# Performance work log

Measured on AMD Instinct MI355X. Metric: run time of the kernel, lower is better.

The kernel has to match this reference:

```python
import jax, jax.numpy as jnp
import numpy as np


def setup_inputs() -> dict:
    key = jax.random.key(0)
    B, N, C, H, W = 2, 512, 256, 128, 224
    ks = jax.random.split(key, 6)
    point_features = jax.random.normal(ks[0], (B, N, C), dtype=jnp.float32)
    gd = jax.random.uniform(ks[1], (B, N, 14), dtype=jnp.float32)
    # realistic radar positions (meters): X in [-10,10], Y in [-2,2], Z (depth) in [1,41]
    pos = jnp.stack([(gd[..., 0] - 0.5) * 20.0,
                     (gd[..., 1] - 0.5) * 4.0,
                     gd[..., 2] * 40.0 + 1.0], axis=-1)
    gd = gd.at[..., :3].set(pos)
    # sigmas in original-image pixels, in [0, 20] so some exceed 1 after scaling
    gd = gd.at[..., 5:7].set(gd[..., 5:7] * 20.0)
    # nuScenes-like intrinsics for a 1600x900 camera
    K = jnp.array([[500.0, 0.0, 800.0], [0.0, 500.0, 450.0], [0.0, 0.0, 1.0]], dtype=jnp.float32)
    intrinsic = jnp.tile(K[None], (B, 1, 1))
    sc = 1.0 / np.sqrt(C)
    W1 = jax.random.normal(ks[2], (C, C), dtype=jnp.float32) * sc
    b1 = jax.random.normal(ks[3], (C,), dtype=jnp.float32) * 0.01
    W2 = jax.random.normal(ks[4], (C, C), dtype=jnp.float32) * sc
    b2 = jax.random.normal(ks[5], (C,), dtype=jnp.float32) * 0.01
    return {"point_features": point_features, "gaussian_data": gd, "intrinsic": intrinsic,
            "W1": W1, "b1": b1, "W2": W2, "b2": b2, "H": H, "W": W}


def reference(point_features, gaussian_data, intrinsic, W1, b1, W2, b2, H, W):
    pf, gd, K = point_features, gaussian_data, intrinsic
    B, N, C = pf.shape
    # positions / sigmas are consumed via numpy/.item() in the original -> constants w.r.t. autodiff
    pos = jax.lax.stop_gradient(gd[..., :3])          # (B,N,3)
    sig_x = jax.lax.stop_gradient(gd[..., 5])         # (B,N)
    sig_y = jax.lax.stop_gradient(gd[..., 6])         # (B,N)
    wts = gd[..., 12]                                  # (B,N) differentiable weights

    valid = pos[..., 2] > 0.1
    # project to image plane
    p2h = jnp.einsum('bij,bnj->bni', K, pos)           # (B,N,3)
    p2 = p2h[..., :2] / (p2h[..., 2:3] + 1e-6)
    scale_x = W / K[:, 0, 2] / 2.0                     # (B,)
    scale_y = H / K[:, 1, 2] / 2.0
    cx = p2[..., 0] * scale_x[:, None]                 # (B,N)
    cy = p2[..., 1] * scale_y[:, None]
    inb = (cx >= 0) & (cx < W) & (cy >= 0) & (cy < H)
    active = (valid & inb).astype(pf.dtype)            # (B,N)

    sxv = jnp.maximum(sig_x * scale_x[:, None], 1.0)   # (B,N)
    syv = jnp.maximum(sig_y * scale_y[:, None], 1.0)

    xs = jnp.arange(W, dtype=pf.dtype)
    ys = jnp.arange(H, dtype=pf.dtype)
    dist_x = ((xs[None, None, :] - cx[..., None]) / sxv[..., None]) ** 2  # (B,N,W)
    dist_y = ((ys[None, None, :] - cy[..., None]) / syv[..., None]) ** 2  # (B,N,H)
    dist = dist_y[..., :, None] + dist_x[..., None, :]                    # (B,N,H,W)
    gw = jnp.exp(-0.5 * dist) * (dist < 9.0).astype(pf.dtype)
    gw = gw * (wts * active)[..., None, None]                             # masked splat weights

    # feature transform: Linear -> ReLU -> Linear
    h = jax.nn.relu(pf @ W1.T + b1) @ W2.T + b2                           # (B,N,C)

    feature_map = jnp.einsum('bnhw,bnc->bchw', gw, h)                     # (B,C,H,W)
    avg_sigma = 0.5 * (sxv + syv)                                         # (B,N)
    uncertainty_map = jnp.einsum('bnhw,bn->bhw', gw, avg_sigma)[:, None]  # (B,1,H,W)
    density_map = jnp.clip(jnp.sum(gw, axis=1), 1e-6, None)[:, None]      # (B,1,H,W)

    return feature_map / density_map, uncertainty_map / density_map, density_map
```

## Files before the change

### kernel.cpp

```cpp
#include <hip/hip_runtime.h>
#include <math.h>

#define PTS 8
#define PX 16
#define CH 8
#define NTX 14
#define NBLK 1536

__global__ void prep_kernel(const float* __restrict__ gd,
                            const float* __restrict__ Kmat,
                            float4* __restrict__ bbox,
                            float4* __restrict__ prm,
                            int N, int B, float Wf, float Hf) {
  int i = blockIdx.x * blockDim.x + threadIdx.x;
  if (i >= B * N) return;
  int b = i / N;
  const float* g = gd + (size_t)i * 14;
  float X = g[0], Y = g[1], Z = g[2];
  float sigx = g[5], sigy = g[6], wt = g[12];
  const float* K = Kmat + (size_t)b * 9;
  float p0 = K[0]*X + K[1]*Y + K[2]*Z;
  float p1 = K[3]*X + K[4]*Y + K[5]*Z;
  float p2 = K[6]*X + K[7]*Y + K[8]*Z;
  float denom = p2 + 1e-6f;
  float p2x = p0 / denom, p2y = p1 / denom;
  float scale_x = Wf / K[2] * 0.5f;
  float scale_y = Hf / K[5] * 0.5f;
  float cx = p2x * scale_x;
  float cy = p2y * scale_y;
  bool valid = Z > 0.1f;
  bool inb = (cx >= 0.f) && (cx < Wf) && (cy >= 0.f) && (cy < Hf);
  bool active = valid && inb;
  float sxv = fmaxf(sigx * scale_x, 1.f);
  float syv = fmaxf(sigy * scale_y, 1.f);
  float wn = active ? wt : 0.f;
  float avg = 0.5f * (sxv + syv);
  if (active && wn != 0.f) {
    bbox[i] = make_float4(cx, cy, 3.f * sxv, 3.f * syv);
  } else {
    bbox[i] = make_float4(-1e30f, -1e30f, 0.f, 0.f);
  }
  prm[i] = make_float4(1.f / sxv, 1.f / syv, wn, avg);
}

__global__ __launch_bounds__(256, 2) void mlp_kernel(
    const float* __restrict__ pf, const float* __restrict__ W1,
    const float* __restrict__ b1, const float* __restrict__ W2,
    const float* __restrict__ b2, float* __restrict__ hout, int npts) {
  const int t = threadIdx.x;
  const int p0 = blockIdx.x * PTS;
  __shared__ __align__(16) float xs[PTS][256];

  const float4* pf4 = (const float4*)(pf + (size_t)p0 * 256);
  float4* xs4 = (float4*)&xs[0][0];
  #pragma unroll
  for (int i = 0; i < PTS * 64 / 256; ++i) xs4[t + 256 * i] = pf4[t + 256 * i];
  __syncthreads();

  float acc[PTS];
  float bb1 = b1[t];
  #pragma unroll
  for (int p = 0; p < PTS; ++p) acc[p] = bb1;
  const float* w1r = W1 + (size_t)t * 256;
  for (int k = 0; k < 256; k += 4) {
    float4 w = *(const float4*)(w1r + k);
    #pragma unroll
    for (int p = 0; p < PTS; ++p) {
      float4 x = *(const float4*)(&xs[p][k]);
      acc[p] += w.x * x.x + w.y * x.y + w.z * x.z + w.w * x.w;
    }
  }
  __syncthreads();
  #pragma unroll
  for (int p = 0; p < PTS; ++p) xs[p][t] = fmaxf(acc[p], 0.f);
  __syncthreads();

  float acc2[PTS];
  float bb2 = b2[t];
  #pragma unroll
  for (int p = 0; p < PTS; ++p) acc2[p] = bb2;
  const float* w2r = W2 + (size_t)t * 256;
  for (int k = 0; k < 256; k += 4) {
    float4 w = *(const float4*)(w2r + k);
    #pragma unroll
    for (int p = 0; p < PTS; ++p) {
      float4 x = *(const float4*)(&xs[p][k]);
      acc2[p] += w.x * x.x + w.y * x.y + w.z * x.z + w.w * x.w;
    }
  }
  #pragma unroll
  for (int p = 0; p < PTS; ++p)
    if (p0 + p < npts) hout[((size_t)(p0 + p)) * 256 + t] = acc2[p];
}

__global__ __launch_bounds__(256) void tilecull_kernel(
    const float4* __restrict__ bbox, int* __restrict__ tilelist,
    int* __restrict__ tilecnt, int N, int H, int W) {
  const int t = threadIdx.x;
  const int row = blockIdx.x;
  const int b = blockIdx.y;
  __shared__ int wcnt[4];
  __shared__ float xlo_s[512], xhi_s[512];
  __shared__ short gid_s[512];
  const float rf = (float)row;
  const float wmax = (float)(W - 1);
  const int lane = t & 63, wave = t >> 6;
  const unsigned long long lmask = (1ull << lane) - 1ull;
  const size_t bN = (size_t)b * N;

  int rowlen = 0;
  for (int gb = 0; gb < N; gb += 256) {
    int g = gb + t;
    bool f = false;
    float bxlo = 0.f, bxhi = 0.f;
    if (g < N) {
      float4 bb = bbox[bN + g];
      bxlo = bb.x - bb.z; bxhi = bb.x + bb.z;
      f = (bb.y - bb.w <= rf) && (bb.y + bb.w >= rf) &&
          (bxhi >= 0.f) && (bxlo <= wmax);
    }
    unsigned long long m = __ballot(f);
    if (lane == 0) wcnt[wave] = __popcll(m);
    __syncthreads();
    int pre = 0;
    #pragma unroll
    for (int wv = 0; wv < 4; ++wv) pre += (wv < wave) ? wcnt[wv] : 0;
    int tot = wcnt[0] + wcnt[1] + wcnt[2] + wcnt[3];
    if (f) {
      int idx = rowlen + pre + __popcll(m & lmask);
      gid_s[idx] = (short)g; xlo_s[idx] = bxlo; xhi_s[idx] = bxhi;
    }
    __syncthreads();
    rowlen += tot;
  }

  for (int tx = wave; tx < NTX; tx += 4) {
    const float txlo = (float)(tx * PX), txhi = txlo + (float)(PX - 1);
    const size_t tid = ((size_t)b * H + row) * NTX + tx;
    int* out = tilelist + tid * 512;
    int cnt = 0;
    for (int rb = 0; rb < rowlen; rb += 64) {
      int i = rb + lane;
      bool f = false; int g = 0;
      if (i < rowlen) {
        f = (xhi_s[i] >= txlo) && (xlo_s[i] <= txhi);
        g = gid_s[i];
      }
      unsigned long long m = __ballot(f);
      if (f) out[cnt + __popcll(m & lmask)] = g;
      cnt += __popcll(m);
    }
    if (lane == 0) tilecnt[tid] = cnt;
  }
}

__global__ __launch_bounds__(256) void splat_kernel(
    const float4* __restrict__ bbox, const float4* __restrict__ prm,
    const float* __restrict__ hfeat,
    const int* __restrict__ tilelist, const int* __restrict__ tilecnt,
    float* __restrict__ fout, float* __restrict__ unc_out,
    float* __restrict__ dens_out, int N, int C, int H, int W, int ntiles) {
  const int t = threadIdx.x;
  const int HW = H * W;

  __shared__ int glist[512];
  __shared__ __align__(16) float wlds[2][CH][PX];
  __shared__ __align__(16) float invd_s[PX];
  __shared__ float avgs_s[2][CH];

  const int cg = t >> 2, pq = t & 3;
  const int gi_w = t >> 4, j_w = t & 15;

  for (int tid = blockIdx.x; tid < ntiles; tid += NBLK) {
    const int tx = tid % NTX;
    const int rowb = tid / NTX;
    const int row = rowb % H;
    const int b = rowb / H;
    const int x0 = tx * PX;
    const size_t bN = (size_t)b * N;
    const float rf = (float)row;
    const float xlo = (float)x0;

    const int cnt = tilecnt[tid];
    __syncthreads();

    if (cnt == 0) {
      if (t < PX) {
        size_t pix = (size_t)b * HW + (size_t)row * W + x0 + t;
        dens_out[pix] = 1e-6f;
        unc_out[pix] = 0.f;
      }
      float4 z = make_float4(0.f, 0.f, 0.f, 0.f);
      float* fo = fout + ((size_t)(b * C + 4 * cg)) * HW + (size_t)row * W + x0 + 4 * pq;
      *(float4*)(fo)        = z;
      *(float4*)(fo + HW)   = z;
      *(float4*)(fo + 2*HW) = z;
      *(float4*)(fo + 3*HW) = z;
      continue;
    }

    for (int i = t; i < cnt; i += 256) glist[i] = tilelist[(size_t)tid * 512 + i];
    __syncthreads();

    float dreg = 0.f, ureg = 0.f;
    float4 a0 = make_float4(0.f,0.f,0.f,0.f), a1 = a0, a2 = a0, a3 = a0;
    float4 hvA[CH], hvB[CH];
    const int nchunk = (cnt + CH - 1) / CH;

#define HV8(HV, CB) do { \
    int gn_ = cnt - (CB); \
    _Pragma("unroll") \
    for (int gi = 0; gi < CH; ++gi) { \
      int idx_ = (CB) + gi; if (idx_ > cnt - 1) idx_ = cnt - 1; \
      HV[gi] = (gi < gn_) ? *(const float4*)(hfeat + (bN + glist[idx_]) * (size_t)C + 4 * cg) \
                          : make_float4(0.f, 0.f, 0.f, 0.f); \
    } } while (0)

#define WGT8(BUF, CB) do { \
    if (t < CH * PX) { \
      float w_ = 0.f, av_ = 0.f; \
      int gn_ = cnt - (CB); \
      if (gi_w < gn_) { \
        int g_ = glist[(CB) + gi_w]; \
        float4 bb_ = bbox[bN + g_]; \
        float4 pr_ = prm[bN + g_]; \
        float dx_ = (xlo + (float)j_w - bb_.x) * pr_.x; \
        float dy_ = (rf - bb_.y) * pr_.y; \
        float q_ = dx_ * dx_ + dy_ * dy_; \
        w_ = (q_ < 9.f) ? __expf(-0.5f * q_) * pr_.z : 0.f; \
        av_ = pr_.w; \
      } \
      wlds[BUF][gi_w][j_w] = w_; \
      if (j_w == 0) avgs_s[BUF][gi_w] = av_; \
    } } while (0)

#define DENS8(BUF, GC) do { \
    if (t < PX) { \
      for (int gi = 0; gi < (GC); ++gi) { \
        float w = wlds[BUF][gi][t]; \
        dreg += w; ureg += w * avgs_s[BUF][gi]; \
      } } } while (0)

#define FMA8(BUF, HV) do { \
    const float4* wr_ = (const float4*)&wlds[BUF][0][0]; \
    _Pragma("unroll") \
    for (int gi = 0; gi < CH; ++gi) { \
      float4 w = wr_[gi * 4 + pq]; \
      float4 h = HV[gi]; \
      a0.x += w.x*h.x; a0.y += w.y*h.x; a0.z += w.z*h.x; a0.w += w.w*h.x; \
      a1.x += w.x*h.y; a1.y += w.y*h.y; a1.z += w.z*h.y; a1.w += w.w*h.y; \
      a2.x += w.x*h.z; a2.y += w.y*h.z; a2.z += w.z*h.z; a2.w += w.w*h.z; \
      a3.x += w.x*h.w; a3.y += w.y*h.w; a3.z += w.z*h.w; a3.w += w.w*h.w; \
    } } while (0)

    HV8(hvA, 0);
    WGT8(0, 0);
    __syncthreads();
    for (int c = 0; c < nchunk; c += 2) {
      {
        const int gc = min(CH, cnt - c * CH);
        HV8(hvB, (c + 1) * CH);
        WGT8(1, (c + 1) * CH);
        DENS8(0, gc);
        FMA8(0, hvA);
        __syncthreads();
      }
      if (c + 1 < nchunk) {
        const int gc = min(CH, cnt - (c + 1) * CH);
        HV8(hvA, (c + 2) * CH);
        WGT8(0, (c + 2) * CH);
        DENS8(1, gc);
        FMA8(1, hvB);
        __syncthreads();
      }
    }

    if (t < PX) {
      float dc = fmaxf(dreg, 1e-6f);
      float inv = 1.f / dc;
      invd_s[t] = inv;
      size_t pix = (size_t)b * HW + (size_t)row * W + x0 + t;
      dens_out[pix] = dc;
      unc_out[pix] = ureg * inv;
    }
    __syncthreads();

    float4 iq = *(const float4*)&invd_s[4 * pq];
    float* fo = fout + ((size_t)(b * C + 4 * cg)) * HW + (size_t)row * W + x0 + 4 * pq;
    *(float4*)(fo)        = make_float4(a0.x*iq.x, a0.y*iq.y, a0.z*iq.z, a0.w*iq.w);
    *(float4*)(fo + HW)   = make_float4(a1.x*iq.x, a1.y*iq.y, a1.z*iq.z, a1.w*iq.w);
    *(float4*)(fo + 2*HW) = make_float4(a2.x*iq.x, a2.y*iq.y, a2.z*iq.z, a2.w*iq.w);
    *(float4*)(fo + 3*HW) = make_float4(a3.x*iq.x, a3.y*iq.y, a3.z*iq.z, a3.w*iq.w);

#undef HV8
#undef WGT8
#undef DENS8
#undef FMA8
  }
}

extern "C" void kernel_launch(void* const* d_in, const int* in_sizes, int n_in,
                              void* d_out, int out_size, void* d_ws, size_t ws_size,
                              hipStream_t stream) {
  const float* pf = (const float*)d_in[0];
  const float* gd = (const float*)d_in[1];
  const float* K  = (const float*)d_in[2];
  const float* W1 = (const float*)d_in[3];
  const float* b1 = (const float*)d_in[4];
  const float* W2 = (const float*)d_in[5];
  const float* b2 = (const float*)d_in[6];

  const int B = in_sizes[2] / 9;
  const int N = in_sizes[1] / (B * 14);
  const int C = in_sizes[0] / (B * N);
  const int H = 128, W = 224;
  const int ntiles = B * H * NTX;

  char* wsb = (char*)d_ws;
  size_t off = 0;
  float4* bbox = (float4*)(wsb + off); off += (size_t)B * N * sizeof(float4);
  float4* prm  = (float4*)(wsb + off); off += (size_t)B * N * sizeof(float4);
  float*  hfe  = (float*)(wsb + off);  off += (size_t)B * N * C * 4;
  int* tilelist = (int*)(wsb + off);   off += (size_t)ntiles * 512 * 4;
  int* tilecnt  = (int*)(wsb + off);   off += (size_t)ntiles * 4;

  float* out      = (float*)d_out;
  float* unc_out  = out + (size_t)B * C * H * W;
  float* dens_out = unc_out + (size_t)B * H * W;

  prep_kernel<<<dim3((B * N + 255) / 256), 256, 0, stream>>>(
      gd, K, bbox, prm, N, B, (float)W, (float)H);
  tilecull_kernel<<<dim3(H, B), 256, 0, stream>>>(
      bbox, tilelist, tilecnt, N, H, W);
  mlp_kernel<<<dim3((B * N + PTS - 1) / PTS), 256, 0, stream>>>(
      pf, W1, b1, W2, b2, hfe, B * N);
  splat_kernel<<<dim3(NBLK), 256, 0, stream>>>(
      bbox, prm, hfe, tilelist, tilecnt, out, unc_out, dens_out,
      N, C, H, W, ntiles);
}
```

Measured before the change: 89.05 us.

## Split splat tiles into channel halves with atomic work queue scheduling

Each splat tile is split into two work units covering 128 channels each, so every thread accumulates two channels instead of four. Blocks now pull units from a global atomic counter instead of a static stride, which balances uneven per-tile gaussian counts. The chunk size grows to 16 gaussians, the block count to 2048, and the MLP uses 4 points per block without the occupancy hint. In exchange, the Gaussian weights are computed twice per tile, once per channel half, and every unit pays an atomic and extra barriers.

Result: slower. 140.5 us (+57.8%).

```diff
diff --git a/kernel.cpp b/kernel.cpp
--- a/kernel.cpp
+++ b/kernel.cpp
@@ -1,11 +1,11 @@
 #include <hip/hip_runtime.h>
 #include <math.h>
 
-#define PTS 8
+#define PTS 4
 #define PX 16
-#define CH 8
+#define CH 16
 #define NTX 14
-#define NBLK 1536
+#define NBLK 2048
 
 __global__ void prep_kernel(const float* __restrict__ gd,
                             const float* __restrict__ Kmat,
@@ -43,7 +43,7 @@
   prm[i] = make_float4(1.f / sxv, 1.f / syv, wn, avg);
 }
 
-__global__ __launch_bounds__(256, 2) void mlp_kernel(
+__global__ __launch_bounds__(256) void mlp_kernel(
     const float* __restrict__ pf, const float* __restrict__ W1,
     const float* __restrict__ b1, const float* __restrict__ W2,
     const float* __restrict__ b2, float* __restrict__ hout, int npts) {
@@ -95,7 +95,8 @@
 
 __global__ __launch_bounds__(256) void tilecull_kernel(
     const float4* __restrict__ bbox, int* __restrict__ tilelist,
-    int* __restrict__ tilecnt, int N, int H, int W) {
+    int* __restrict__ tilecnt, int* __restrict__ qhead,
+    int N, int H, int W) {
   const int t = threadIdx.x;
   const int row = blockIdx.x;
   const int b = blockIdx.y;
@@ -107,6 +108,8 @@
   const int lane = t & 63, wave = t >> 6;
   const unsigned long long lmask = (1ull << lane) - 1ull;
   const size_t bN = (size_t)b * N;
+
+  if (t == 0 && row == 0 && b == 0) *qhead = NBLK;
 
   int rowlen = 0;
   for (int gb = 0; gb < N; gb += 256) {
@@ -158,8 +161,9 @@
     const float4* __restrict__ bbox, const float4* __restrict__ prm,
     const float* __restrict__ hfeat,
     const int* __restrict__ tilelist, const int* __restrict__ tilecnt,
+    int* __restrict__ qhead,
     float* __restrict__ fout, float* __restrict__ unc_out,
-    float* __restrict__ dens_out, int N, int C, int H, int W, int ntiles) {
+    float* __restrict__ dens_out, int N, int C, int H, int W, int nunits) {
   const int t = threadIdx.x;
   const int HW = H * W;
 
@@ -167,135 +171,137 @@
   __shared__ __align__(16) float wlds[2][CH][PX];
   __shared__ __align__(16) float invd_s[PX];
   __shared__ float avgs_s[2][CH];
+  __shared__ int unit_s;
 
   const int cg = t >> 2, pq = t & 3;
   const int gi_w = t >> 4, j_w = t & 15;
 
-  for (int tid = blockIdx.x; tid < ntiles; tid += NBLK) {
-    const int tx = tid % NTX;
-    const int rowb = tid / NTX;
+  int unit = blockIdx.x;
+  while (unit < nunits) {
+    const int tileid = unit >> 1;
+    const int chh = unit & 1;
+    const int tx = tileid % NTX;
+    const int rowb = tileid / NTX;
     const int row = rowb % H;
     const int b = rowb / H;
     const int x0 = tx * PX;
+    const int chbase = chh << 7;
     const size_t bN = (size_t)b * N;
     const float rf = (float)row;
     const float xlo = (float)x0;
-
-    const int cnt = tilecnt[tid];
-    __syncthreads();
+    const int cnt = tilecnt[tileid];
+
+    float* fo = fout + ((size_t)(b * C + chbase + 2 * cg)) * HW
+                     + (size_t)row * W + x0 + 4 * pq;
 
     if (cnt == 0) {
-      if (t < PX) {
+      if (chh == 0 && t < PX) {
         size_t pix = (size_t)b * HW + (size_t)row * W + x0 + t;
         dens_out[pix] = 1e-6f;
         unc_out[pix] = 0.f;
       }
       float4 z = make_float4(0.f, 0.f, 0.f, 0.f);
-      float* fo = fout + ((size_t)(b * C + 4 * cg)) * HW + (size_t)row * W + x0 + 4 * pq;
-      *(float4*)(fo)        = z;
-      *(float4*)(fo + HW)   = z;
-      *(float4*)(fo + 2*HW) = z;
-      *(float4*)(fo + 3*HW) = z;
-      continue;
-    }
-
-    for (int i = t; i < cnt; i += 256) glist[i] = tilelist[(size_t)tid * 512 + i];
-    __syncthreads();
-
-    float dreg = 0.f, ureg = 0.f;
-    float4 a0 = make_float4(0.f,0.f,0.f,0.f), a1 = a0, a2 = a0, a3 = a0;
-    float4 hvA[CH], hvB[CH];
-    const int nchunk = (cnt + CH - 1) / CH;
-
-#define HV8(HV, CB) do { \
+      *(float4*)(fo)      = z;
+      *(float4*)(fo + HW) = z;
+    } else {
+      for (int i = t; i < cnt; i += 256) glist[i] = tilelist[(size_t)tileid * 512 + i];
+      __syncthreads();
+
+      float dreg = 0.f, ureg = 0.f;
+      float4 a0 = make_float4(0.f, 0.f, 0.f, 0.f), a1 = a0;
+      float2 hvA[CH], hvB[CH];
+      const int nchunk = (cnt + CH - 1) / CH;
+
+#define HV16(HV, CB) do { \
     int gn_ = cnt - (CB); \
     _Pragma("unroll") \
     for (int gi = 0; gi < CH; ++gi) { \
       int idx_ = (CB) + gi; if (idx_ > cnt - 1) idx_ = cnt - 1; \
-      HV[gi] = (gi < gn_) ? *(const float4*)(hfeat + (bN + glist[idx_]) * (size_t)C + 4 * cg) \
-                          : make_float4(0.f, 0.f, 0.f, 0.f); \
+      HV[gi] = (gi < gn_) ? *(const float2*)(hfeat + (bN + glist[idx_]) * (size_t)C + chbase + 2 * cg) \
+                          : make_float2(0.f, 0.f); \
     } } while (0)
 
-#define WGT8(BUF, CB) do { \
-    if (t < CH * PX) { \
-      float w_ = 0.f, av_ = 0.f; \
-      int gn_ = cnt - (CB); \
-      if (gi_w < gn_) { \
-        int g_ = glist[(CB) + gi_w]; \
-        float4 bb_ = bbox[bN + g_]; \
-        float4 pr_ = prm[bN + g_]; \
-        float dx_ = (xlo + (float)j_w - bb_.x) * pr_.x; \
-        float dy_ = (rf - bb_.y) * pr_.y; \
-        float q_ = dx_ * dx_ + dy_ * dy_; \
-        w_ = (q_ < 9.f) ? __expf(-0.5f * q_) * pr_.z : 0.f; \
-        av_ = pr_.w; \
-      } \
-      wlds[BUF][gi_w][j_w] = w_; \
-      if (j_w == 0) avgs_s[BUF][gi_w] = av_; \
-    } } while (0)
-
-#define DENS8(BUF, GC) do { \
+#define WGT16(BUF, CB) do { \
+    float w_ = 0.f, av_ = 0.f; \
+    int gn_ = cnt - (CB); \
+    if (gi_w < gn_) { \
+      int g_ = glist[(CB) + gi_w]; \
+      float4 bb_ = bbox[bN + g_]; \
+      float4 pr_ = prm[bN + g_]; \
+      float dx_ = (xlo + (float)j_w - bb_.x) * pr_.x; \
+      float dy_ = (rf - bb_.y) * pr_.y; \
+      float q_ = dx_ * dx_ + dy_ * dy_; \
+      w_ = (q_ < 9.f) ? __expf(-0.5f * q_) * pr_.z : 0.f; \
+      av_ = pr_.w; \
+    } \
+    wlds[BUF][gi_w][j_w] = w_; \
+    if (j_w == 0) avgs_s[BUF][gi_w] = av_; } while (0)
+
+#define DENS16(BUF, GC) do { \
     if (t < PX) { \
       for (int gi = 0; gi < (GC); ++gi) { \
         float w = wlds[BUF][gi][t]; \
         dreg += w; ureg += w * avgs_s[BUF][gi]; \
       } } } while (0)
 
-#define FMA8(BUF, HV) do { \
+#define FMA16(BUF, HV) do { \
     const float4* wr_ = (const float4*)&wlds[BUF][0][0]; \
     _Pragma("unroll") \
     for (int gi = 0; gi < CH; ++gi) { \
       float4 w = wr_[gi * 4 + pq]; \
-      float4 h = HV[gi]; \
+      float2 h = HV[gi]; \
       a0.x += w.x*h.x; a0.y += w.y*h.x; a0.z += w.z*h.x; a0.w += w.w*h.x; \
       a1.x += w.x*h.y; a1.y += w.y*h.y; a1.z += w.z*h.y; a1.w += w.w*h.y; \
-      a2.x += w.x*h.z; a2.y += w.y*h.z; a2.z += w.z*h.z; a2.w += w.w*h.z; \
-      a3.x += w.x*h.w; a3.y += w.y*h.w; a3.z += w.z*h.w; a3.w += w.w*h.w; \
     } } while (0)
 
-    HV8(hvA, 0);
-    WGT8(0, 0);
+      HV16(hvA, 0);
+      WGT16(0, 0);
+      __syncthreads();
+      for (int c = 0; c < nchunk; c += 2) {
+        {
+          const int gc = min(CH, cnt - c * CH);
+          HV16(hvB, (c + 1) * CH);
+          WGT16(1, (c + 1) * CH);
+          DENS16(0, gc);
+          FMA16(0, hvA);
+          __syncthreads();
+        }
+        if (c + 1 < nchunk) {
+          const int gc = min(CH, cnt - (c + 1) * CH);
+          HV16(hvA, (c + 2) * CH);
+          WGT16(0, (c + 2) * CH);
+          DENS16(1, gc);
+          FMA16(1, hvB);
+          __syncthreads();
+        }
+      }
+
+      if (t < PX) {
+        float dc = fmaxf(dreg, 1e-6f);
+        float inv = 1.f / dc;
+        invd_s[t] = inv;
+        if (chh == 0) {
+          size_t pix = (size_t)b * HW + (size_t)row * W + x0 + t;
+          dens_out[pix] = dc;
+          unc_out[pix] = ureg * inv;
+        }
+      }
+      __syncthreads();
+
+      float4 iq = *(const float4*)&invd_s[4 * pq];
+      *(float4*)(fo)      = make_float4(a0.x*iq.x, a0.y*iq.y, a0.z*iq.z, a0.w*iq.w);
+      *(float4*)(fo + HW) = make_float4(a1.x*iq.x, a1.y*iq.y, a1.z*iq.z, a1.w*iq.w);
+
+#undef HV16
+#undef WGT16
+#undef DENS16
+#undef FMA16
+    }
+
     __syncthreads();
-    for (int c = 0; c < nchunk; c += 2) {
-      {
-        const int gc = min(CH, cnt - c * CH);
-        HV8(hvB, (c + 1) * CH);
-        WGT8(1, (c + 1) * CH);
-        DENS8(0, gc);
-        FMA8(0, hvA);
-        __syncthreads();
-      }
-      if (c + 1 < nchunk) {
-        const int gc = min(CH, cnt - (c + 1) * CH);
-        HV8(hvA, (c + 2) * CH);
-        WGT8(0, (c + 2) * CH);
-        DENS8(1, gc);
-        FMA8(1, hvB);
-        __syncthreads();
-      }
-    }
-
-    if (t < PX) {
-      float dc = fmaxf(dreg, 1e-6f);
-      float inv = 1.f / dc;
-      invd_s[t] = inv;
-      size_t pix = (size_t)b * HW + (size_t)row * W + x0 + t;
-      dens_out[pix] = dc;
-      unc_out[pix] = ureg * inv;
-    }
+    if (t == 0) unit_s = atomicAdd(qhead, 1);
     __syncthreads();
-
-    float4 iq = *(const float4*)&invd_s[4 * pq];
-    float* fo = fout + ((size_t)(b * C + 4 * cg)) * HW + (size_t)row * W + x0 + 4 * pq;
-    *(float4*)(fo)        = make_float4(a0.x*iq.x, a0.y*iq.y, a0.z*iq.z, a0.w*iq.w);
-    *(float4*)(fo + HW)   = make_float4(a1.x*iq.x, a1.y*iq.y, a1.z*iq.z, a1.w*iq.w);
-    *(float4*)(fo + 2*HW) = make_float4(a2.x*iq.x, a2.y*iq.y, a2.z*iq.z, a2.w*iq.w);
-    *(float4*)(fo + 3*HW) = make_float4(a3.x*iq.x, a3.y*iq.y, a3.z*iq.z, a3.w*iq.w);
-
-#undef HV8
-#undef WGT8
-#undef DENS8
-#undef FMA8
+    unit = unit_s;
   }
 }
 
@@ -315,6 +321,7 @@
   const int C = in_sizes[0] / (B * N);
   const int H = 128, W = 224;
   const int ntiles = B * H * NTX;
+  const int nunits = ntiles * 2;
 
   char* wsb = (char*)d_ws;
   size_t off = 0;
@@ -323,6 +330,7 @@
   float*  hfe  = (float*)(wsb + off);  off += (size_t)B * N * C * 4;
   int* tilelist = (int*)(wsb + off);   off += (size_t)ntiles * 512 * 4;
   int* tilecnt  = (int*)(wsb + off);   off += (size_t)ntiles * 4;
+  int* qhead    = (int*)(wsb + off);   off += 16;
 
   float* out      = (float*)d_out;
   float* unc_out  = out + (size_t)B * C * H * W;
@@ -331,10 +339,10 @@
   prep_kernel<<<dim3((B * N + 255) / 256), 256, 0, stream>>>(
       gd, K, bbox, prm, N, B, (float)W, (float)H);
   tilecull_kernel<<<dim3(H, B), 256, 0, stream>>>(
-      bbox, tilelist, tilecnt, N, H, W);
+      bbox, tilelist, tilecnt, qhead, N, H, W);
   mlp_kernel<<<dim3((B * N + PTS - 1) / PTS), 256, 0, stream>>>(
       pf, W1, b1, W2, b2, hfe, B * N);
   splat_kernel<<<dim3(NBLK), 256, 0, stream>>>(
-      bbox, prm, hfe, tilelist, tilecnt, out, unc_out, dens_out,
-      N, C, H, W, ntiles);
-}
+      bbox, prm, hfe, tilelist, tilecnt, qhead, out, unc_out, dens_out,
+      N, C, H, W, nunits);
+}
```
